# Performance work log

Hardware: AMD Instinct MI355X
Metric: run time of the kernel (lower is better)

The kernel has to match this reference:

```python
import jax, jax.numpy as jnp
import numpy as np

SOFTMAX_TEMP = 0.01
CART_PIXEL_WIDTH = 256
CART_RESOLUTION = 0.2592


def zn_desc(desc):
    # desc: B x C x N. Zero-mean, unit-std over channel dim (torch.std default ddof=1).
    mean = jnp.mean(desc, axis=1, keepdims=True)
    std = jnp.std(desc, axis=1, keepdims=True, ddof=1)
    return (desc - mean) / std


def compute_2D_from_3D(coords):
    cart_min_range = (CART_PIXEL_WIDTH / 2 - 0.5) * CART_RESOLUTION
    u = (cart_min_range + coords[:, 1]) / CART_RESOLUTION
    v = (cart_min_range - coords[:, 0]) / CART_RESOLUTION
    return jnp.stack([u, v], axis=2)


def setup_inputs() -> dict:
    key = jax.random.key(0)
    B, C, N, H, W = 2, 256, 1024, 256, 256
    ks = jax.random.split(key, 4)
    tgt_coords = jax.random.normal(ks[0], (B, 3, H * W), jnp.float32) * 10.0
    tgt_weights = jax.random.uniform(ks[1], (B, 1, H, W), dtype=jnp.float32)
    src_desc_norm = zn_desc(jax.random.normal(ks[2], (B, C, N), jnp.float32))
    tgt_desc = jax.random.normal(ks[3], (B, C, H, W), jnp.float32)
    return {
        'geometry_img': jnp.zeros((1,), jnp.int32),
        'tgt_coords': tgt_coords,
        'tgt_2D': jnp.zeros((1,), jnp.int32),
        'tgt_weights': tgt_weights,
        'tgt_weights_dense': jnp.zeros((1,), jnp.int32),
        'src_desc_norm': src_desc_norm,
        'tgt_desc': tgt_desc,
        'tgt_desc_dense': jnp.zeros((1,), jnp.int32),
        'cam_calib': jnp.zeros((1,), jnp.int32),
        'window_size': 16,
    }


def reference(geometry_img, tgt_coords, tgt_2D, tgt_weights, tgt_weights_dense,
              src_desc_norm, tgt_desc, tgt_desc_dense, cam_calib, window_size):
    B, C = tgt_desc.shape[0], tgt_desc.shape[1]
    M = tgt_desc.shape[2] * tgt_desc.shape[3]
    N = src_desc_norm.shape[2]

    tgt_desc_flat = tgt_desc.reshape(B, C, M)
    tgt_desc_norm = zn_desc(tgt_desc_flat)

    # B x N x M similarity (ZNCC): src^T @ tgt / C
    match_vals = jnp.einsum('bcn,bcm->bnm', src_desc_norm, tgt_desc_norm) / float(C)
    soft_match_vals = jax.nn.softmax(match_vals / SOFTMAX_TEMP, axis=2)
    max_softmax = jnp.max(soft_match_vals, axis=(1, 2))  # (B,)

    # three weighted sums sharing the same softmax matrix
    pseudo_coords = jnp.einsum('bcm,bnm->bcn', tgt_coords, soft_match_vals)
    pseudo_weights = jnp.einsum('bcm,bnm->bcn', tgt_weights.reshape(B, 1, M), soft_match_vals)
    pseudo_descs = jnp.einsum('bcm,bnm->bcn', tgt_desc_flat, soft_match_vals)          # B x C x N

    pseudo_2D = compute_2D_from_3D(pseudo_coords)  # B x N x 2
    pseudo_descs = zn_desc(pseudo_descs)
    valid_pts = jnp.ones((B, 1, N), jnp.int32)
    return pseudo_coords, pseudo_weights, pseudo_descs, pseudo_2D, valid_pts, max_softmax
```

## Files before the change

### kernel.cpp

```cpp
#include <hip/hip_runtime.h>
#include <hip/hip_bf16.h>

#define Bb   2
#define Cc   256
#define Nn   1024
#define Mm   65536
#define MCn  16
#define VROWS 272
#define MSTEP 32
#define MCHUNK (Mm / MCn)
#define NIT  (MCHUNK / MSTEP)

#define SCL_OFF  0L
#define TMC_OFF  524288L
#define TCM_OFF  67633152L
#define SNC_OFF  138936320L
#define PART_OFF 139984896L
#define ZP_OFF   157810688L
#define PP_OFF   157941760L
#define PS_OFF   PART_OFF
#define PS2_OFF  (PART_OFF + 2097152L)

#define O_COORD 0L
#define O_W     6144L
#define O_DESC  8192L
#define O_P2D   532480L
#define O_VALID 536576L
#define O_MAXSM 538624L

using f32x4 = __attribute__((ext_vector_type(4))) float;
using s16x8 = __attribute__((ext_vector_type(8))) short;

__device__ inline unsigned short f2bf(float x) {
    union { float f; unsigned int u; } v; v.f = x;
    unsigned int r = v.u + 0x7FFFu + ((v.u >> 16) & 1u);
    return (unsigned short)(r >> 16);
}
__device__ inline float bf2f(unsigned short u) {
    union { unsigned int u; float f; } v; v.u = ((unsigned int)u) << 16;
    return v.f;
}
__device__ inline float exp2v(float x) {
    float r; asm("v_exp_f32 %0, %1" : "=v"(r) : "v"(x)); return r;
}
__device__ inline unsigned int cvtpk(float lo, float hi) {
    unsigned int r;
    asm("v_cvt_pk_bf16_f32 %0, %1, %2" : "=v"(r) : "v"(lo), "v"(hi));
    return r;
}

__device__ inline void gld_lds16(const unsigned short* g, unsigned short* l) {
    __builtin_amdgcn_global_load_lds(
        (const __attribute__((address_space(1))) unsigned int*)g,
        (__attribute__((address_space(3))) unsigned int*)l, 16, 0, 0);
}

__global__ void k_prep_tgt(const float* __restrict__ tgt,
                           unsigned short* __restrict__ tmc,
                           unsigned short* __restrict__ tcm,
                           float* __restrict__ ps,
                           float* __restrict__ ps2) {
    __shared__ float lds[64][65];
    __shared__ float sm[4][64], sm2[4][64];
    int b = blockIdx.z, cy = blockIdx.y, c0 = cy * 64;
    long m0 = (long)blockIdx.x * 64;
    int ty = threadIdx.x >> 6, tx = threadIdx.x & 63;
    float s = 0.f, s2 = 0.f;
    #pragma unroll
    for (int k = 0; k < 16; ++k) {
        int ci = 4 * k + ty;
        float v = tgt[((long)b * Cc + c0 + ci) * Mm + m0 + tx];
        lds[ci][tx] = v;
        s += v; s2 += v * v;
        tcm[((long)b * VROWS + c0 + ci) * Mm + m0 + tx] = f2bf(v);
    }
    sm[ty][tx] = s; sm2[ty][tx] = s2;
    __syncthreads();
    #pragma unroll
    for (int k = 0; k < 16; ++k) {
        int mi = 4 * k + ty;
        tmc[((long)b * Mm + m0 + mi) * Cc + c0 + tx] = f2bf(lds[tx][mi]);
    }
    if (ty == 0) {
        long o = ((long)b * 4 + cy) * Mm + m0 + tx;
        ps[o]  = (sm[0][tx] + sm[1][tx]) + (sm[2][tx] + sm[3][tx]);
        ps2[o] = (sm2[0][tx] + sm2[1][tx]) + (sm2[2][tx] + sm2[3][tx]);
    }
}

__global__ void k_stats(const float* __restrict__ ps,
                        const float* __restrict__ ps2,
                        const float* __restrict__ coords,
                        const float* __restrict__ weights,
                        float* __restrict__ scl,
                        unsigned short* __restrict__ tcm) {
    int b = blockIdx.y;
    long m = (long)blockIdx.x * 256 + threadIdx.x;
    float s = 0.f, s2 = 0.f;
    #pragma unroll
    for (int k = 0; k < 4; ++k) {
        long o = ((long)b * 4 + k) * Mm + m;
        s += ps[o]; s2 += ps2[o];
    }
    float var = fmaxf((s2 - s * s * (1.0f / Cc)) * (1.0f / (Cc - 1)), 1e-20f);
    scl[(long)b * Mm + m] = 1.4426950408889634f * rsqrtf(var) * (1.0f / (Cc * 0.01f));
    unsigned short* vrow = tcm + ((long)b * VROWS + 256) * Mm + m;
    #pragma unroll
    for (int i = 0; i < 3; ++i) vrow[(long)i * Mm] = f2bf(coords[((long)b * 3 + i) * Mm + m]);
    vrow[3L * Mm] = f2bf(weights[(long)b * Mm + m]);
    vrow[4L * Mm] = 0x3F80;
    #pragma unroll
    for (int i = 5; i < 16; ++i) vrow[(long)i * Mm] = 0;
}

__global__ void k_prep_src(const float* __restrict__ src, unsigned short* __restrict__ snc) {
    __shared__ float lds[64][65];
    int b = blockIdx.z, c0 = blockIdx.y * 64, n0 = blockIdx.x * 64;
    int ty = threadIdx.x >> 6, tx = threadIdx.x & 63;
    #pragma unroll
    for (int k = 0; k < 16; ++k)
        lds[4 * k + ty][tx] = src[((long)b * Cc + c0 + 4 * k + ty) * Nn + n0 + tx];
    __syncthreads();
    #pragma unroll
    for (int k = 0; k < 16; ++k) {
        int ni = 4 * k + ty;
        snc[((long)b * Nn + n0 + ni) * Cc + c0 + tx] = f2bf(lds[tx][ni]);
    }
}

__global__ __launch_bounds__(256, 1) void k_main(const unsigned short* __restrict__ tmc,
                                                 const unsigned short* __restrict__ tcm,
                                                 const unsigned short* __restrict__ snc,
                                                 const float* __restrict__ scl,
                                                 unsigned short* __restrict__ part,
                                                 float* __restrict__ zp,
                                                 float* __restrict__ pp) {
    __shared__ __align__(16) unsigned short kb0[8192], kb1[8192];
    __shared__ __align__(16) unsigned short vb0[8704], vb1[8704];
    __shared__ __align__(16) unsigned short pbuf[4][2][16][56];

    int w = threadIdx.x >> 6, lane = threadIdx.x & 63;
    int l15 = lane & 15, lg = lane >> 4;
    int b = blockIdx.z, nt = blockIdx.y, mc = blockIdx.x;
    int nb = nt * 128 + w * 32;
    long mbase = (long)mc * MCHUNK;

    s16x8 qf[2][8];
    #pragma unroll
    for (int st = 0; st < 2; ++st) {
        const unsigned short* qp = snc + ((long)b * Nn + nb + st * 16 + l15) * Cc + lg * 8;
        #pragma unroll
        for (int cc = 0; cc < 8; ++cc) qf[st][cc] = *(const s16x8*)(qp + cc * 32);
    }

    f32x4 acc[2][17];
    #pragma unroll
    for (int st = 0; st < 2; ++st)
        #pragma unroll
        for (int t = 0; t < 17; ++t) acc[st][t] = (f32x4){0.f, 0.f, 0.f, 0.f};
    float pmax[2] = {0.f, 0.f};

    const unsigned short* tmcb = tmc + (long)b * Mm * Cc;
    const unsigned short* tcmb = tcm + (long)b * VROWS * (long)Mm;
    const unsigned short* ksrc[4];
    #pragma unroll
    for (int i = 0; i < 4; ++i) {
        int ins = w * 4 + i;
        int row = 2 * ins + (lane >> 5);
        int gs  = (lane & 31) ^ (row & 7);
        ksrc[i] = tmcb + (mbase + row) * Cc + gs * 8;
    }
    const unsigned short* vsrc[5];
    int vj = ((lane & 3) ^ ((lane >> 3) & 3)) * 8;
    #pragma unroll
    for (int i = 0; i < 5; ++i) {
        int ins = (i < 4) ? (w * 4 + i) : 16;
        int row = ins * 16 + (lane >> 2);
        vsrc[i] = tcmb + (long)row * Mm + mbase + vj;
    }

    const float* sclb = scl + (long)b * Mm;

    auto stage = [&](int d) {
        unsigned short* kd = d ? kb1 : kb0;
        unsigned short* vd = d ? vb1 : vb0;
        #pragma unroll
        for (int i = 0; i < 4; ++i) gld_lds16(ksrc[i], kd + (w * 4 + i) * 512);
        #pragma unroll
        for (int i = 0; i < 4; ++i) gld_lds16(vsrc[i], vd + (w * 4 + i) * 512);
        if (w == 3) gld_lds16(vsrc[4], vd + 16 * 512);
    };
    auto advance = [&]() {
        #pragma unroll
        for (int i = 0; i < 4; ++i) ksrc[i] += MSTEP * Cc;
        #pragma unroll
        for (int i = 0; i < 5; ++i) vsrc[i] += MSTEP;
    };

    stage(0);
    advance();
    __syncthreads();

    int ksw = (l15 & 7) << 3;
    int vsw = (lg ^ ((l15 >> 1) & 3)) * 8;

    float4 scA = *(const float4*)(sclb + mbase + lg * 4);
    float4 scB = *(const float4*)(sclb + mbase + 16 + lg * 4);

    for (int s = 0; s < NIT; ++s) {
        int cur = s & 1;
        if (s + 1 < NIT) { stage(cur ^ 1); advance(); }
        const unsigned short* kbc = cur ? kb1 : kb0;
        const unsigned short* vbc = cur ? vb1 : vb0;
        int sn = (s + 1 < NIT) ? s + 1 : s;
        float4 nA = *(const float4*)(sclb + mbase + (long)sn * MSTEP + lg * 4);
        float4 nB = *(const float4*)(sclb + mbase + (long)sn * MSTEP + 16 + lg * 4);

        #pragma unroll
        for (int t = 0; t < 2; ++t) {
            f32x4 dA = (f32x4){0.f, 0.f, 0.f, 0.f};
            f32x4 dB = (f32x4){0.f, 0.f, 0.f, 0.f};
            const unsigned short* kr = kbc + (t * 16 + l15) * Cc;
            #pragma unroll
            for (int cc = 0; cc < 8; ++cc) {
                s16x8 kf = *(const s16x8*)(kr + ((cc * 32 + lg * 8) ^ ksw));
                dA = __builtin_amdgcn_mfma_f32_16x16x32_bf16(kf, qf[0][cc], dA, 0, 0, 0);
                dB = __builtin_amdgcn_mfma_f32_16x16x32_bf16(kf, qf[1][cc], dB, 0, 0, 0);
            }
            float4 sc = t ? scB : scA;
            #pragma unroll
            for (int st = 0; st < 2; ++st) {
                f32x4 d = st ? dB : dA;
                float p0 = exp2v(d.x * sc.x);
                float p1 = exp2v(d.y * sc.y);
                float p2 = exp2v(d.z * sc.z);
                float p3 = exp2v(d.w * sc.w);
                pmax[st] = fmaxf(pmax[st], fmaxf(fmaxf(p0, p1), fmaxf(p2, p3)));
                unsigned long long pk =
                    (unsigned long long)cvtpk(p0, p1) | ((unsigned long long)cvtpk(p2, p3) << 32);
                *(unsigned long long*)&pbuf[w][st][l15][t * 16 + lg * 4] = pk;
            }
        }
        s16x8 pfA = *(const s16x8*)&pbuf[w][0][l15][lg * 8];
        s16x8 pfB = *(const s16x8*)&pbuf[w][1][l15][lg * 8];
        #pragma unroll
        for (int t = 0; t < 17; ++t) {
            s16x8 vf = *(const s16x8*)(vbc + (t * 16 + l15) * MSTEP + vsw);
            acc[0][t] = __builtin_amdgcn_mfma_f32_16x16x32_bf16(vf, pfA, acc[0][t], 0, 0, 0);
            acc[1][t] = __builtin_amdgcn_mfma_f32_16x16x32_bf16(vf, pfB, acc[1][t], 0, 0, 0);
        }
        scA = nA; scB = nB;
        __syncthreads();
    }

    #pragma unroll
    for (int st = 0; st < 2; ++st) {
        float pt = fmaxf(pmax[st], __shfl_xor(pmax[st], 16));
        pt = fmaxf(pt, __shfl_xor(pt, 32));
        long zi = ((long)(b * MCn + mc)) * Nn + nb + st * 16;
        if (lg == 1) zp[zi + l15] = acc[st][16].x;
        if (lane < 16) pp[zi + lane] = pt;
        unsigned short* po = part + (((long)(b * MCn + mc) * Nn) + nb + st * 16 + l15) * VROWS;
        #pragma unroll
        for (int t = 0; t < 17; ++t) {
            f32x4 a = acc[st][t];
            unsigned long long pk =
                (unsigned long long)cvtpk(a.x, a.y) | ((unsigned long long)cvtpk(a.z, a.w) << 32);
            *(unsigned long long*)&po[t * 16 + lg * 4] = pk;
        }
    }
}

__global__ void k_epi(const unsigned short* __restrict__ part,
                      const float* __restrict__ zp,
                      const float* __restrict__ pp,
                      float* __restrict__ out) {
    int w = threadIdx.x >> 6, lane = threadIdx.x & 63;
    int bn = blockIdx.x * 4 + w;
    int b = bn >> 10, n = bn & 1023;

    float Z = 0.f, pm = 0.f;
    #pragma unroll
    for (int mc = 0; mc < MCn; ++mc) {
        long zi = ((long)(b * MCn + mc)) * Nn + n;
        Z += zp[zi];
        pm = fmaxf(pm, pp[zi]);
    }
    float invZ = 1.0f / Z;

    float dv[4], s1 = 0.f, s2 = 0.f;
    #pragma unroll
    for (int k = 0; k < 4; ++k) {
        int c = lane + 64 * k;
        float s = 0.f;
        #pragma unroll
        for (int mc = 0; mc < MCn; ++mc)
            s += bf2f(part[((long)(b * MCn + mc) * Nn + n) * VROWS + c]);
        float d = s * invZ;
        dv[k] = d; s1 += d; s2 += d * d;
    }
    #pragma unroll
    for (int off = 1; off < 64; off <<= 1) { s1 += __shfl_xor(s1, off); s2 += __shfl_xor(s2, off); }
    float mean = s1 * (1.0f / 256.0f);
    float var = fmaxf((s2 - 256.0f * mean * mean) * (1.0f / 255.0f), 1e-20f);
    float istd = 1.0f / sqrtf(var);
    #pragma unroll
    for (int k = 0; k < 4; ++k)
        out[O_DESC + ((long)b * Cc + lane + 64 * k) * Nn + n] = (dv[k] - mean) * istd;

    float ex = 0.f;
    if (lane < 4) {
        int c = 256 + lane;
        #pragma unroll
        for (int mc = 0; mc < MCn; ++mc)
            ex += bf2f(part[((long)(b * MCn + mc) * Nn + n) * VROWS + c]);
        ex *= invZ;
    }
    float pc0 = __shfl(ex, 0), pc1 = __shfl(ex, 1), pc2 = __shfl(ex, 2), wv = __shfl(ex, 3);
    if (lane == 0) {
        out[O_COORD + ((long)b * 3 + 0) * Nn + n] = pc0;
        out[O_COORD + ((long)b * 3 + 1) * Nn + n] = pc1;
        out[O_COORD + ((long)b * 3 + 2) * Nn + n] = pc2;
        out[O_W + (long)b * Nn + n] = wv;
        const float cmin = 33.048f;
        out[O_P2D + ((long)b * Nn + n) * 2 + 0] = (cmin + pc1) * (1.0f / 0.2592f);
        out[O_P2D + ((long)b * Nn + n) * 2 + 1] = (cmin - pc0) * (1.0f / 0.2592f);
        out[O_VALID + (long)b * Nn + n] = 1.0f;
        atomicMax((unsigned int*)out + O_MAXSM + b, __float_as_uint(pm * invZ));
    }
}

extern "C" void kernel_launch(void* const* d_in, const int* in_sizes, int n_in,
                              void* d_out, int out_size, void* d_ws, size_t ws_size,
                              hipStream_t stream) {
    const float* tgt_coords  = (const float*)d_in[1];
    const float* tgt_weights = (const float*)d_in[3];
    const float* src_desc    = (const float*)d_in[5];
    const float* tgt_desc    = (const float*)d_in[6];

    char* ws = (char*)d_ws;
    float* scl           = (float*)(ws + SCL_OFF);
    unsigned short* tmc  = (unsigned short*)(ws + TMC_OFF);
    unsigned short* tcm  = (unsigned short*)(ws + TCM_OFF);
    unsigned short* snc  = (unsigned short*)(ws + SNC_OFF);
    unsigned short* part = (unsigned short*)(ws + PART_OFF);
    float* ps            = (float*)(ws + PS_OFF);
    float* ps2           = (float*)(ws + PS2_OFF);
    float* zp            = (float*)(ws + ZP_OFF);
    float* pp            = (float*)(ws + PP_OFF);
    float* out           = (float*)d_out;

    k_prep_tgt<<<dim3(Mm / 64, Cc / 64, Bb), 256, 0, stream>>>(tgt_desc, tmc, tcm, ps, ps2);
    k_stats<<<dim3(Mm / 256, Bb), 256, 0, stream>>>(ps, ps2, tgt_coords, tgt_weights, scl, tcm);
    k_prep_src<<<dim3(Nn / 64, Cc / 64, Bb), 256, 0, stream>>>(src_desc, snc);
    k_main<<<dim3(MCn, Nn / 128, Bb), 256, 0, stream>>>(tmc, tcm, snc, scl, part, zp, pp);
    hipMemsetAsync((char*)d_out + O_MAXSM * 4, 0, 2 * sizeof(float), stream);
    k_epi<<<dim3((Bb * Nn) / 4), 256, 0, stream>>>(part, zp, pp, out);
}
```

Before: 336.6 us.

## Software-pipeline QK and PV stages with triple-buffered V and double-buffered P

Restructures the main loop so that iteration s computes the QK scores and exponentials for step s while running the PV MFMAs on the probabilities from step s-1. V tiles get a third LDS buffer and the P buffer is double-buffered so the lagged PV can read data that is not being overwritten. A tail block finishes the last PV step. The intent is to overlap the exp/convert work with the matrix ops and break the per-iteration dependency, at the cost of extra LDS, which may reduce occupancy.

```diff
diff --git a/kernel.cpp b/kernel.cpp
--- a/kernel.cpp
+++ b/kernel.cpp
@@ -136,8 +136,8 @@
                                                  float* __restrict__ zp,
                                                  float* __restrict__ pp) {
     __shared__ __align__(16) unsigned short kb0[8192], kb1[8192];
-    __shared__ __align__(16) unsigned short vb0[8704], vb1[8704];
-    __shared__ __align__(16) unsigned short pbuf[4][2][16][56];
+    __shared__ __align__(16) unsigned short vb0[8704], vb1[8704], vb2[8704];
+    __shared__ __align__(16) unsigned short pbuf[2][4][2][16][56];
 
     int w = threadIdx.x >> 6, lane = threadIdx.x & 63;
     int l15 = lane & 15, lg = lane >> 4;
@@ -181,9 +181,7 @@
 
     const float* sclb = scl + (long)b * Mm;
 
-    auto stage = [&](int d) {
-        unsigned short* kd = d ? kb1 : kb0;
-        unsigned short* vd = d ? vb1 : vb0;
+    auto stage = [&](unsigned short* kd, unsigned short* vd) {
         #pragma unroll
         for (int i = 0; i < 4; ++i) gld_lds16(ksrc[i], kd + (w * 4 + i) * 512);
         #pragma unroll
@@ -197,7 +195,10 @@
         for (int i = 0; i < 5; ++i) vsrc[i] += MSTEP;
     };
 
-    stage(0);
+    unsigned short *kc = kb0, *kn = kb1;
+    unsigned short *vp = vb2, *vc = vb0, *vn = vb1;
+
+    stage(kc, vc);
     advance();
     __syncthreads();
 
@@ -208,19 +209,17 @@
     float4 scB = *(const float4*)(sclb + mbase + 16 + lg * 4);
 
     for (int s = 0; s < NIT; ++s) {
-        int cur = s & 1;
-        if (s + 1 < NIT) { stage(cur ^ 1); advance(); }
-        const unsigned short* kbc = cur ? kb1 : kb0;
-        const unsigned short* vbc = cur ? vb1 : vb0;
+        if (s + 1 < NIT) { stage(kn, vn); advance(); }
         int sn = (s + 1 < NIT) ? s + 1 : s;
         float4 nA = *(const float4*)(sclb + mbase + (long)sn * MSTEP + lg * 4);
         float4 nB = *(const float4*)(sclb + mbase + (long)sn * MSTEP + 16 + lg * 4);
 
+        unsigned short* pw = &pbuf[s & 1][w][0][0][0];
         #pragma unroll
         for (int t = 0; t < 2; ++t) {
             f32x4 dA = (f32x4){0.f, 0.f, 0.f, 0.f};
             f32x4 dB = (f32x4){0.f, 0.f, 0.f, 0.f};
-            const unsigned short* kr = kbc + (t * 16 + l15) * Cc;
+            const unsigned short* kr = kc + (t * 16 + l15) * Cc;
             #pragma unroll
             for (int cc = 0; cc < 8; ++cc) {
                 s16x8 kf = *(const s16x8*)(kr + ((cc * 32 + lg * 8) ^ ksw));
@@ -238,19 +237,38 @@
                 pmax[st] = fmaxf(pmax[st], fmaxf(fmaxf(p0, p1), fmaxf(p2, p3)));
                 unsigned long long pk =
                     (unsigned long long)cvtpk(p0, p1) | ((unsigned long long)cvtpk(p2, p3) << 32);
-                *(unsigned long long*)&pbuf[w][st][l15][t * 16 + lg * 4] = pk;
+                *(unsigned long long*)(pw + (st * 16 + l15) * 56 + t * 16 + lg * 4) = pk;
             }
         }
-        s16x8 pfA = *(const s16x8*)&pbuf[w][0][l15][lg * 8];
-        s16x8 pfB = *(const s16x8*)&pbuf[w][1][l15][lg * 8];
+
+        if (s) {
+            const unsigned short* pr = &pbuf[(s & 1) ^ 1][w][0][0][0];
+            s16x8 pfA = *(const s16x8*)(pr + l15 * 56 + lg * 8);
+            s16x8 pfB = *(const s16x8*)(pr + (16 + l15) * 56 + lg * 8);
+            #pragma unroll
+            for (int t = 0; t < 17; ++t) {
+                s16x8 vf = *(const s16x8*)(vp + (t * 16 + l15) * MSTEP + vsw);
+                acc[0][t] = __builtin_amdgcn_mfma_f32_16x16x32_bf16(vf, pfA, acc[0][t], 0, 0, 0);
+                acc[1][t] = __builtin_amdgcn_mfma_f32_16x16x32_bf16(vf, pfB, acc[1][t], 0, 0, 0);
+            }
+        }
+
+        scA = nA; scB = nB;
+        __syncthreads();
+        unsigned short* kt = kc; kc = kn; kn = kt;
+        unsigned short* vt = vp; vp = vc; vc = vn; vn = vt;
+    }
+
+    {
+        const unsigned short* pr = &pbuf[(NIT - 1) & 1][w][0][0][0];
+        s16x8 pfA = *(const s16x8*)(pr + l15 * 56 + lg * 8);
+        s16x8 pfB = *(const s16x8*)(pr + (16 + l15) * 56 + lg * 8);
         #pragma unroll
         for (int t = 0; t < 17; ++t) {
-            s16x8 vf = *(const s16x8*)(vbc + (t * 16 + l15) * MSTEP + vsw);
+            s16x8 vf = *(const s16x8*)(vp + (t * 16 + l15) * MSTEP + vsw);
             acc[0][t] = __builtin_amdgcn_mfma_f32_16x16x32_bf16(vf, pfA, acc[0][t], 0, 0, 0);
             acc[1][t] = __builtin_amdgcn_mfma_f32_16x16x32_bf16(vf, pfB, acc[1][t], 0, 0, 0);
         }
-        scA = nA; scB = nB;
-        __syncthreads();
     }
 
     #pragma unroll
```

Measured after the change: 324.9 us. 1.04x faster.

## Use 512-thread blocks sharing K/V tiles and reduce partials with float atomics

Applied to the files above, without the earlier changes.

Each main-kernel block now has 8 wavefronts covering 256 source points, so every staged K/V tile in LDS is reused across twice as many rows. The M dimension is split into 32 chunks to keep the grid size. Per-chunk bf16 partials are replaced by fp32 atomicAdd into a single zeroed accumulator, plus atomicMax for the softmax peak. This removes the multi-chunk reduction from the epilogue but adds atomic traffic, a memset, and register pressure from launch_bounds(512,2).

```diff
diff --git a/kernel.cpp b/kernel.cpp
--- a/kernel.cpp
+++ b/kernel.cpp
@@ -5,7 +5,7 @@
 #define Cc   256
 #define Nn   1024
 #define Mm   65536
-#define MCn  16
+#define MCn  32
 #define VROWS 272
 #define MSTEP 32
 #define MCHUNK (Mm / MCn)
@@ -15,11 +15,11 @@
 #define TMC_OFF  524288L
 #define TCM_OFF  67633152L
 #define SNC_OFF  138936320L
-#define PART_OFF 139984896L
-#define ZP_OFF   157810688L
-#define PP_OFF   157941760L
-#define PS_OFF   PART_OFF
-#define PS2_OFF  (PART_OFF + 2097152L)
+#define PARTF_OFF 139984896L
+#define PPM_OFF   142213120L
+#define PS_OFF    142221312L
+#define PS2_OFF   144318464L
+#define ZERO_BYTES 2236416L
 
 #define O_COORD 0L
 #define O_W     6144L
@@ -35,10 +35,6 @@
     union { float f; unsigned int u; } v; v.f = x;
     unsigned int r = v.u + 0x7FFFu + ((v.u >> 16) & 1u);
     return (unsigned short)(r >> 16);
-}
-__device__ inline float bf2f(unsigned short u) {
-    union { unsigned int u; float f; } v; v.u = ((unsigned int)u) << 16;
-    return v.f;
 }
 __device__ inline float exp2v(float x) {
     float r; asm("v_exp_f32 %0, %1" : "=v"(r) : "v"(x)); return r;
@@ -128,21 +124,20 @@
     }
 }
 
-__global__ __launch_bounds__(256, 1) void k_main(const unsigned short* __restrict__ tmc,
+__global__ __launch_bounds__(512, 2) void k_main(const unsigned short* __restrict__ tmc,
                                                  const unsigned short* __restrict__ tcm,
                                                  const unsigned short* __restrict__ snc,
                                                  const float* __restrict__ scl,
-                                                 unsigned short* __restrict__ part,
-                                                 float* __restrict__ zp,
-                                                 float* __restrict__ pp) {
+                                                 float* __restrict__ partf,
+                                                 unsigned int* __restrict__ ppmax) {
     __shared__ __align__(16) unsigned short kb0[8192], kb1[8192];
     __shared__ __align__(16) unsigned short vb0[8704], vb1[8704];
-    __shared__ __align__(16) unsigned short pbuf[4][2][16][56];
+    __shared__ __align__(16) unsigned short pbuf[8][2][16][40];
 
     int w = threadIdx.x >> 6, lane = threadIdx.x & 63;
     int l15 = lane & 15, lg = lane >> 4;
     int b = blockIdx.z, nt = blockIdx.y, mc = blockIdx.x;
-    int nb = nt * 128 + w * 32;
+    int nb = nt * 256 + w * 32;
     long mbase = (long)mc * MCHUNK;
 
     s16x8 qf[2][8];
@@ -162,19 +157,19 @@
 
     const unsigned short* tmcb = tmc + (long)b * Mm * Cc;
     const unsigned short* tcmb = tcm + (long)b * VROWS * (long)Mm;
-    const unsigned short* ksrc[4];
-    #pragma unroll
-    for (int i = 0; i < 4; ++i) {
-        int ins = w * 4 + i;
+    const unsigned short* ksrc[2];
+    #pragma unroll
+    for (int i = 0; i < 2; ++i) {
+        int ins = 2 * w + i;
         int row = 2 * ins + (lane >> 5);
         int gs  = (lane & 31) ^ (row & 7);
         ksrc[i] = tmcb + (mbase + row) * Cc + gs * 8;
     }
-    const unsigned short* vsrc[5];
+    const unsigned short* vsrc[3];
     int vj = ((lane & 3) ^ ((lane >> 3) & 3)) * 8;
     #pragma unroll
-    for (int i = 0; i < 5; ++i) {
-        int ins = (i < 4) ? (w * 4 + i) : 16;
+    for (int i = 0; i < 3; ++i) {
+        int ins = (i < 2) ? (2 * w + i) : 16;
         int row = ins * 16 + (lane >> 2);
         vsrc[i] = tcmb + (long)row * Mm + mbase + vj;
     }
@@ -185,16 +180,16 @@
         unsigned short* kd = d ? kb1 : kb0;
         unsigned short* vd = d ? vb1 : vb0;
         #pragma unroll
-        for (int i = 0; i < 4; ++i) gld_lds16(ksrc[i], kd + (w * 4 + i) * 512);
-        #pragma unroll
-        for (int i = 0; i < 4; ++i) gld_lds16(vsrc[i], vd + (w * 4 + i) * 512);
-        if (w == 3) gld_lds16(vsrc[4], vd + 16 * 512);
+        for (int i = 0; i < 2; ++i) gld_lds16(ksrc[i], kd + (2 * w + i) * 512);
+        #pragma unroll
+        for (int i = 0; i < 2; ++i) gld_lds16(vsrc[i], vd + (2 * w + i) * 512);
+        if (w == 7) gld_lds16(vsrc[2], vd + 16 * 512);
     };
     auto advance = [&]() {
         #pragma unroll
-        for (int i = 0; i < 4; ++i) ksrc[i] += MSTEP * Cc;
-        #pragma unroll
-        for (int i = 0; i < 5; ++i) vsrc[i] += MSTEP;
+        for (int i = 0; i < 2; ++i) ksrc[i] += MSTEP * Cc;
+        #pragma unroll
+        for (int i = 0; i < 3; ++i) vsrc[i] += MSTEP;
     };
 
     stage(0);
@@ -203,18 +198,13 @@
 
     int ksw = (l15 & 7) << 3;
     int vsw = (lg ^ ((l15 >> 1) & 3)) * 8;
-
-    float4 scA = *(const float4*)(sclb + mbase + lg * 4);
-    float4 scB = *(const float4*)(sclb + mbase + 16 + lg * 4);
 
     for (int s = 0; s < NIT; ++s) {
         int cur = s & 1;
         if (s + 1 < NIT) { stage(cur ^ 1); advance(); }
         const unsigned short* kbc = cur ? kb1 : kb0;
         const unsigned short* vbc = cur ? vb1 : vb0;
-        int sn = (s + 1 < NIT) ? s + 1 : s;
-        float4 nA = *(const float4*)(sclb + mbase + (long)sn * MSTEP + lg * 4);
-        float4 nB = *(const float4*)(sclb + mbase + (long)sn * MSTEP + 16 + lg * 4);
+        long m0 = mbase + (long)s * MSTEP;
 
         #pragma unroll
         for (int t = 0; t < 2; ++t) {
@@ -227,7 +217,7 @@
                 dA = __builtin_amdgcn_mfma_f32_16x16x32_bf16(kf, qf[0][cc], dA, 0, 0, 0);
                 dB = __builtin_amdgcn_mfma_f32_16x16x32_bf16(kf, qf[1][cc], dB, 0, 0, 0);
             }
-            float4 sc = t ? scB : scA;
+            float4 sc = *(const float4*)(sclb + m0 + t * 16 + lg * 4);
             #pragma unroll
             for (int st = 0; st < 2; ++st) {
                 f32x4 d = st ? dB : dA;
@@ -249,7 +239,6 @@
             acc[0][t] = __builtin_amdgcn_mfma_f32_16x16x32_bf16(vf, pfA, acc[0][t], 0, 0, 0);
             acc[1][t] = __builtin_amdgcn_mfma_f32_16x16x32_bf16(vf, pfB, acc[1][t], 0, 0, 0);
         }
-        scA = nA; scB = nB;
         __syncthreads();
     }
 
@@ -257,46 +246,35 @@
     for (int st = 0; st < 2; ++st) {
         float pt = fmaxf(pmax[st], __shfl_xor(pmax[st], 16));
         pt = fmaxf(pt, __shfl_xor(pt, 32));
-        long zi = ((long)(b * MCn + mc)) * Nn + nb + st * 16;
-        if (lg == 1) zp[zi + l15] = acc[st][16].x;
-        if (lane < 16) pp[zi + lane] = pt;
-        unsigned short* po = part + (((long)(b * MCn + mc) * Nn) + nb + st * 16 + l15) * VROWS;
+        if (lane < 16)
+            atomicMax(ppmax + (long)b * Nn + nb + st * 16 + lane, __float_as_uint(pt));
+        float* po = partf + ((long)b * Nn + nb + st * 16 + l15) * VROWS;
         #pragma unroll
         for (int t = 0; t < 17; ++t) {
             f32x4 a = acc[st][t];
-            unsigned long long pk =
-                (unsigned long long)cvtpk(a.x, a.y) | ((unsigned long long)cvtpk(a.z, a.w) << 32);
-            *(unsigned long long*)&po[t * 16 + lg * 4] = pk;
+            atomicAdd(&po[t * 16 + lg * 4 + 0], a.x);
+            atomicAdd(&po[t * 16 + lg * 4 + 1], a.y);
+            atomicAdd(&po[t * 16 + lg * 4 + 2], a.z);
+            atomicAdd(&po[t * 16 + lg * 4 + 3], a.w);
         }
     }
 }
 
-__global__ void k_epi(const unsigned short* __restrict__ part,
-                      const float* __restrict__ zp,
-                      const float* __restrict__ pp,
+__global__ void k_epi(const float* __restrict__ partf,
+                      const unsigned int* __restrict__ ppmax,
                       float* __restrict__ out) {
     int w = threadIdx.x >> 6, lane = threadIdx.x & 63;
     int bn = blockIdx.x * 4 + w;
     int b = bn >> 10, n = bn & 1023;
 
-    float Z = 0.f, pm = 0.f;
-    #pragma unroll
-    for (int mc = 0; mc < MCn; ++mc) {
-        long zi = ((long)(b * MCn + mc)) * Nn + n;
-        Z += zp[zi];
-        pm = fmaxf(pm, pp[zi]);
-    }
+    const float* pr = partf + (long)bn * VROWS;
+    float Z = pr[260];
     float invZ = 1.0f / Z;
 
     float dv[4], s1 = 0.f, s2 = 0.f;
     #pragma unroll
     for (int k = 0; k < 4; ++k) {
-        int c = lane + 64 * k;
-        float s = 0.f;
-        #pragma unroll
-        for (int mc = 0; mc < MCn; ++mc)
-            s += bf2f(part[((long)(b * MCn + mc) * Nn + n) * VROWS + c]);
-        float d = s * invZ;
+        float d = pr[lane + 64 * k] * invZ;
         dv[k] = d; s1 += d; s2 += d * d;
     }
     #pragma unroll
@@ -308,16 +286,9 @@
     for (int k = 0; k < 4; ++k)
         out[O_DESC + ((long)b * Cc + lane + 64 * k) * Nn + n] = (dv[k] - mean) * istd;
 
-    float ex = 0.f;
-    if (lane < 4) {
-        int c = 256 + lane;
-        #pragma unroll
-        for (int mc = 0; mc < MCn; ++mc)
-            ex += bf2f(part[((long)(b * MCn + mc) * Nn + n) * VROWS + c]);
-        ex *= invZ;
-    }
-    float pc0 = __shfl(ex, 0), pc1 = __shfl(ex, 1), pc2 = __shfl(ex, 2), wv = __shfl(ex, 3);
     if (lane == 0) {
+        float pc0 = pr[256] * invZ, pc1 = pr[257] * invZ, pc2 = pr[258] * invZ;
+        float wv = pr[259] * invZ;
         out[O_COORD + ((long)b * 3 + 0) * Nn + n] = pc0;
         out[O_COORD + ((long)b * 3 + 1) * Nn + n] = pc1;
         out[O_COORD + ((long)b * 3 + 2) * Nn + n] = pc2;
@@ -326,7 +297,8 @@
         out[O_P2D + ((long)b * Nn + n) * 2 + 0] = (cmin + pc1) * (1.0f / 0.2592f);
         out[O_P2D + ((long)b * Nn + n) * 2 + 1] = (cmin - pc0) * (1.0f / 0.2592f);
         out[O_VALID + (long)b * Nn + n] = 1.0f;
-        atomicMax((unsigned int*)out + O_MAXSM + b, __float_as_uint(pm * invZ));
+        float pm = __uint_as_float(ppmax[bn]) * invZ;
+        atomicMax((unsigned int*)out + O_MAXSM + b, __float_as_uint(pm));
     }
 }
 
@@ -343,17 +315,17 @@
     unsigned short* tmc  = (unsigned short*)(ws + TMC_OFF);
     unsigned short* tcm  = (unsigned short*)(ws + TCM_OFF);
     unsigned short* snc  = (unsigned short*)(ws + SNC_OFF);
-    unsigned short* part = (unsigned short*)(ws + PART_OFF);
+    float* partf         = (float*)(ws + PARTF_OFF);
+    unsigned int* ppmax  = (unsigned int*)(ws + PPM_OFF);
     float* ps            = (float*)(ws + PS_OFF);
     float* ps2           = (float*)(ws + PS2_OFF);
-    float* zp            = (float*)(ws + ZP_OFF);
-    float* pp            = (float*)(ws + PP_OFF);
     float* out           = (float*)d_out;
 
     k_prep_tgt<<<dim3(Mm / 64, Cc / 64, Bb), 256, 0, stream>>>(tgt_desc, tmc, tcm, ps, ps2);
     k_stats<<<dim3(Mm / 256, Bb), 256, 0, stream>>>(ps, ps2, tgt_coords, tgt_weights, scl, tcm);
     k_prep_src<<<dim3(Nn / 64, Cc / 64, Bb), 256, 0, stream>>>(src_desc, snc);
-    k_main<<<dim3(MCn, Nn / 128, Bb), 256, 0, stream>>>(tmc, tcm, snc, scl, part, zp, pp);
+    hipMemsetAsync(ws + PARTF_OFF, 0, ZERO_BYTES, stream);
     hipMemsetAsync((char*)d_out + O_MAXSM * 4, 0, 2 * sizeof(float), stream);
-    k_epi<<<dim3((Bb * Nn) / 4), 256, 0, stream>>>(part, zp, pp, out);
-}
+    k_main<<<dim3(MCn, Nn / 256, Bb), 512, 0, stream>>>(tmc, tcm, snc, scl, partf, ppmax);
+    k_epi<<<dim3((Bb * Nn) / 4), 256, 0, stream>>>(partf, ppmax, out);
+}
```

Measured after the change: 457.2 us. +35.8%, slower.

## Load K tiles directly to registers and software-pipeline QK with PV

Applied to the files above, without the earlier changes.

K tiles are no longer staged through LDS. Each lane loads its K fragments straight from global memory into double-buffered registers one step ahead. The V buffer becomes triple-buffered and the P buffer double-buffered, so the PV matmul for step s-1 runs in the same iteration as the QK matmul and softmax for step s, with one barrier per step. This cuts LDS traffic and shortens the dependency chain within each iteration, at the cost of many more live registers (four K fragment arrays) and uncoalesced, strided global loads for K.

```diff
diff --git a/kernel.cpp b/kernel.cpp
--- a/kernel.cpp
+++ b/kernel.cpp
@@ -135,9 +135,8 @@
                                                  unsigned short* __restrict__ part,
                                                  float* __restrict__ zp,
                                                  float* __restrict__ pp) {
-    __shared__ __align__(16) unsigned short kb0[8192], kb1[8192];
-    __shared__ __align__(16) unsigned short vb0[8704], vb1[8704];
-    __shared__ __align__(16) unsigned short pbuf[4][2][16][56];
+    __shared__ __align__(16) unsigned short vb[3][8704];
+    __shared__ __align__(16) unsigned short pbuf[2][4][2][16][40];
 
     int w = threadIdx.x >> 6, lane = threadIdx.x & 63;
     int l15 = lane & 15, lg = lane >> 4;
@@ -161,15 +160,10 @@
     float pmax[2] = {0.f, 0.f};
 
     const unsigned short* tmcb = tmc + (long)b * Mm * Cc;
+    const unsigned short* kt0 = tmcb + (mbase + l15) * Cc + lg * 8;
+    const unsigned short* kt1 = tmcb + (mbase + 16 + l15) * Cc + lg * 8;
+
     const unsigned short* tcmb = tcm + (long)b * VROWS * (long)Mm;
-    const unsigned short* ksrc[4];
-    #pragma unroll
-    for (int i = 0; i < 4; ++i) {
-        int ins = w * 4 + i;
-        int row = 2 * ins + (lane >> 5);
-        int gs  = (lane & 31) ^ (row & 7);
-        ksrc[i] = tmcb + (mbase + row) * Cc + gs * 8;
-    }
     const unsigned short* vsrc[5];
     int vj = ((lane & 3) ^ ((lane >> 3) & 3)) * 8;
     #pragma unroll
@@ -181,77 +175,91 @@
 
     const float* sclb = scl + (long)b * Mm;
 
-    auto stage = [&](int d) {
-        unsigned short* kd = d ? kb1 : kb0;
-        unsigned short* vd = d ? vb1 : vb0;
-        #pragma unroll
-        for (int i = 0; i < 4; ++i) gld_lds16(ksrc[i], kd + (w * 4 + i) * 512);
+    auto stagev = [&](unsigned short* vd) {
         #pragma unroll
         for (int i = 0; i < 4; ++i) gld_lds16(vsrc[i], vd + (w * 4 + i) * 512);
         if (w == 3) gld_lds16(vsrc[4], vd + 16 * 512);
-    };
-    auto advance = [&]() {
-        #pragma unroll
-        for (int i = 0; i < 4; ++i) ksrc[i] += MSTEP * Cc;
         #pragma unroll
         for (int i = 0; i < 5; ++i) vsrc[i] += MSTEP;
     };
-
-    stage(0);
-    advance();
-    __syncthreads();
-
-    int ksw = (l15 & 7) << 3;
+    auto load_k = [&](s16x8* d0, s16x8* d1) {
+        #pragma unroll
+        for (int cc = 0; cc < 8; ++cc) {
+            d0[cc] = *(const s16x8*)(kt0 + cc * 32);
+            d1[cc] = *(const s16x8*)(kt1 + cc * 32);
+        }
+        kt0 += MSTEP * Cc;
+        kt1 += MSTEP * Cc;
+    };
+
     int vsw = (lg ^ ((l15 >> 1) & 3)) * 8;
 
-    float4 scA = *(const float4*)(sclb + mbase + lg * 4);
-    float4 scB = *(const float4*)(sclb + mbase + 16 + lg * 4);
-
-    for (int s = 0; s < NIT; ++s) {
-        int cur = s & 1;
-        if (s + 1 < NIT) { stage(cur ^ 1); advance(); }
-        const unsigned short* kbc = cur ? kb1 : kb0;
-        const unsigned short* vbc = cur ? vb1 : vb0;
-        int sn = (s + 1 < NIT) ? s + 1 : s;
-        float4 nA = *(const float4*)(sclb + mbase + (long)sn * MSTEP + lg * 4);
-        float4 nB = *(const float4*)(sclb + mbase + (long)sn * MSTEP + 16 + lg * 4);
-
-        #pragma unroll
-        for (int t = 0; t < 2; ++t) {
-            f32x4 dA = (f32x4){0.f, 0.f, 0.f, 0.f};
-            f32x4 dB = (f32x4){0.f, 0.f, 0.f, 0.f};
-            const unsigned short* kr = kbc + (t * 16 + l15) * Cc;
-            #pragma unroll
-            for (int cc = 0; cc < 8; ++cc) {
-                s16x8 kf = *(const s16x8*)(kr + ((cc * 32 + lg * 8) ^ ksw));
-                dA = __builtin_amdgcn_mfma_f32_16x16x32_bf16(kf, qf[0][cc], dA, 0, 0, 0);
-                dB = __builtin_amdgcn_mfma_f32_16x16x32_bf16(kf, qf[1][cc], dB, 0, 0, 0);
-            }
-            float4 sc = t ? scB : scA;
-            #pragma unroll
-            for (int st = 0; st < 2; ++st) {
-                f32x4 d = st ? dB : dA;
-                float p0 = exp2v(d.x * sc.x);
-                float p1 = exp2v(d.y * sc.y);
-                float p2 = exp2v(d.z * sc.z);
-                float p3 = exp2v(d.w * sc.w);
-                pmax[st] = fmaxf(pmax[st], fmaxf(fmaxf(p0, p1), fmaxf(p2, p3)));
-                unsigned long long pk =
-                    (unsigned long long)cvtpk(p0, p1) | ((unsigned long long)cvtpk(p2, p3) << 32);
-                *(unsigned long long*)&pbuf[w][st][l15][t * 16 + lg * 4] = pk;
-            }
-        }
-        s16x8 pfA = *(const s16x8*)&pbuf[w][0][l15][lg * 8];
-        s16x8 pfB = *(const s16x8*)&pbuf[w][1][l15][lg * 8];
+    float4 scA, scB;
+
+    auto qk_half = [&](const s16x8* kf, int t, float4 sc, unsigned short* pw) {
+        f32x4 dA = (f32x4){0.f, 0.f, 0.f, 0.f};
+        f32x4 dB = (f32x4){0.f, 0.f, 0.f, 0.f};
+        #pragma unroll
+        for (int cc = 0; cc < 8; ++cc) {
+            dA = __builtin_amdgcn_mfma_f32_16x16x32_bf16(kf[cc], qf[0][cc], dA, 0, 0, 0);
+            dB = __builtin_amdgcn_mfma_f32_16x16x32_bf16(kf[cc], qf[1][cc], dB, 0, 0, 0);
+        }
+        #pragma unroll
+        for (int st = 0; st < 2; ++st) {
+            f32x4 d = st ? dB : dA;
+            float p0 = exp2v(d.x * sc.x);
+            float p1 = exp2v(d.y * sc.y);
+            float p2 = exp2v(d.z * sc.z);
+            float p3 = exp2v(d.w * sc.w);
+            pmax[st] = fmaxf(pmax[st], fmaxf(fmaxf(p0, p1), fmaxf(p2, p3)));
+            unsigned long long pk =
+                (unsigned long long)cvtpk(p0, p1) | ((unsigned long long)cvtpk(p2, p3) << 32);
+            *(unsigned long long*)(pw + (st * 16 + l15) * 40 + t * 16 + lg * 4) = pk;
+        }
+    };
+    auto pv_step = [&](const unsigned short* vbc, const unsigned short* pr) {
+        s16x8 pfA = *(const s16x8*)(pr + l15 * 40 + lg * 8);
+        s16x8 pfB = *(const s16x8*)(pr + (16 + l15) * 40 + lg * 8);
         #pragma unroll
         for (int t = 0; t < 17; ++t) {
             s16x8 vf = *(const s16x8*)(vbc + (t * 16 + l15) * MSTEP + vsw);
             acc[0][t] = __builtin_amdgcn_mfma_f32_16x16x32_bf16(vf, pfA, acc[0][t], 0, 0, 0);
             acc[1][t] = __builtin_amdgcn_mfma_f32_16x16x32_bf16(vf, pfB, acc[1][t], 0, 0, 0);
         }
+    };
+
+    s16x8 kA0[8], kA1[8], kB0[8], kB1[8];
+
+    stagev(vb[0]);
+    load_k(kA0, kA1);
+    scA = *(const float4*)(sclb + mbase + lg * 4);
+    scB = *(const float4*)(sclb + mbase + 16 + lg * 4);
+    __syncthreads();
+
+    auto body = [&](int s, const s16x8* kc0, const s16x8* kc1, s16x8* kn0, s16x8* kn1) {
+        if (s + 1 < NIT) {
+            stagev(vb[(s + 1) % 3]);
+            load_k(kn0, kn1);
+        }
+        int sn = (s + 1 < NIT) ? s + 1 : s;
+        float4 nA = *(const float4*)(sclb + mbase + (long)sn * MSTEP + lg * 4);
+        float4 nB = *(const float4*)(sclb + mbase + (long)sn * MSTEP + 16 + lg * 4);
+
+        unsigned short* pw = &pbuf[s & 1][w][0][0][0];
+        qk_half(kc0, 0, scA, pw);
+        qk_half(kc1, 1, scB, pw);
+
+        if (s) pv_step(vb[(s + 2) % 3], &pbuf[(s & 1) ^ 1][w][0][0][0]);
+
         scA = nA; scB = nB;
         __syncthreads();
-    }
+    };
+
+    for (int s = 0; s < NIT; s += 2) {
+        body(s,     kA0, kA1, kB0, kB1);
+        body(s + 1, kB0, kB1, kA0, kA1);
+    }
+    pv_step(vb[(NIT - 1) % 3], &pbuf[(NIT - 1) & 1][w][0][0][0]);
 
     #pragma unroll
     for (int st = 0; st < 2; ++st) {
@@ -354,6 +362,6 @@
     k_stats<<<dim3(Mm / 256, Bb), 256, 0, stream>>>(ps, ps2, tgt_coords, tgt_weights, scl, tcm);
     k_prep_src<<<dim3(Nn / 64, Cc / 64, Bb), 256, 0, stream>>>(src_desc, snc);
     k_main<<<dim3(MCn, Nn / 128, Bb), 256, 0, stream>>>(tmc, tcm, snc, scl, part, zp, pp);
-    hipMemsetAsync((char*)d_out + O_MAXSM * 4, 0, 2 * sizeof(float), stream);
+    (void)hipMemsetAsync((char*)d_out + O_MAXSM * 4, 0, 2 * sizeof(float), stream);
     k_epi<<<dim3((Bb * Nn) / 4), 256, 0, stream>>>(part, zp, pp, out);
 }
```

Result: slower. 428.1 us (+27.2%).
